# Kernel optimization log

Hardware: AMD Instinct MI355X
Metric: run time of the kernel (lower is better)

## Reference

```python
import jax, jax.numpy as jnp
import numpy as np
import math

EMBED_DIM = 1024
NUM_HEADS = 16
HEAD_DIM = EMBED_DIM // NUM_HEADS


def setup_inputs() -> dict:
    key = jax.random.key(0)
    ks = jax.random.split(key, 11)
    B, S, D = 4, 2048, EMBED_DIM
    scale = 1.0 / math.sqrt(D)
    inp = {
        'q': jax.random.normal(ks[0], (B, S, D), dtype=jnp.float32),
        'k': jax.random.normal(ks[1], (B, S, D), dtype=jnp.float32),
        'v': jax.random.normal(ks[2], (B, S, D), dtype=jnp.float32),
        'Wq': jax.random.normal(ks[3], (D, D), dtype=jnp.float32) * scale,
        'bq': jnp.zeros((D,), dtype=jnp.float32),
        'Wk': jax.random.normal(ks[4], (D, D), dtype=jnp.float32) * scale,
        'bk': jnp.zeros((D,), dtype=jnp.float32),
        'Wv': jax.random.normal(ks[5], (D, D), dtype=jnp.float32) * scale,
        'bv': jnp.zeros((D,), dtype=jnp.float32),
        'Wo': jax.random.normal(ks[6], (D, D), dtype=jnp.float32) * scale,
        'bo': jnp.zeros((D,), dtype=jnp.float32),
    }
    return inp


def reference(q, k, v, Wq, bq, Wk, bk, Wv, bv, Wo, bo):
    B, S, D = q.shape
    H, Hd = NUM_HEADS, HEAD_DIM
    # QKV projections (nn.Linear: x @ W.T + b), split into heads -> [B,H,S,Hd]
    qh = (q @ Wq.T + bq).reshape(B, S, H, Hd).transpose(0, 2, 1, 3)
    kh = (k @ Wk.T + bk).reshape(B, S, H, Hd).transpose(0, 2, 1, 3)
    vh = (v @ Wv.T + bv).reshape(B, S, H, Hd).transpose(0, 2, 1, 3)
    # Scaled dot-product attention, full [B,H,S,S] scores as in source
    scores = jnp.einsum('bhqd,bhkd->bhqk', qh, kh) / math.sqrt(Hd)
    probs = jax.nn.softmax(scores, axis=-1)
    attn = jnp.einsum('bhqk,bhkd->bhqd', probs, vh)
    # Merge heads and output projection
    concat = attn.transpose(0, 2, 1, 3).reshape(B, S, D)
    return concat @ Wo.T + bo
```

## Files before the change

kernel.cpp:

```cpp
#include <hip/hip_runtime.h>
#include <hip/hip_bf16.h>
#include <math.h>

#define D_MODEL 1024
#define NHEADS  16
#define HDIM    64
#define BATCH   4
#define SEQ     2048

typedef __attribute__((ext_vector_type(8))) short short8;
typedef __attribute__((ext_vector_type(4))) float f32x4;

__device__ __forceinline__ short bf16_of(float f) {
  __hip_bfloat16 h = __float2bfloat16(f);
  return *reinterpret_cast<short*>(&h);
}

__device__ __forceinline__ unsigned pack2(float lo, float hi) {
  return (unsigned)(unsigned short)bf16_of(lo) |
         ((unsigned)(unsigned short)bf16_of(hi) << 16);
}

__device__ __forceinline__ short8 mk_frag(unsigned a, unsigned b, unsigned c, unsigned d) {
  union { unsigned u[4]; short8 s; } t;
  t.u[0] = a; t.u[1] = b; t.u[2] = c; t.u[3] = d;
  return t.s;
}

__device__ __forceinline__ float fast_exp2(float x) {
  float r;
  asm("v_exp_f32 %0, %1" : "=v"(r) : "v"(x));
  return r;
}

__device__ __forceinline__ void gload16(const void* g, void* l) {
  __builtin_amdgcn_global_load_lds((const __attribute__((address_space(1))) void*)g,
                                   (__attribute__((address_space(3))) void*)l, 16, 0, 0);
}

__global__ __launch_bounds__(256) void cvt7(
    const float* __restrict__ Wq, const float* __restrict__ Wk,
    const float* __restrict__ Wv, const float* __restrict__ Wo,
    const float* __restrict__ q,  const float* __restrict__ k,
    const float* __restrict__ v,
    short* __restrict__ wdst, short* __restrict__ qc,
    short* __restrict__ kc,   short* __restrict__ vc)
{
  const int w = blockIdx.y;
  const float* s;
  short* d;
  int n4;
  if (w < 4) {
    s = (w == 0) ? Wq : (w == 1) ? Wk : (w == 2) ? Wv : Wo;
    d = wdst + (size_t)w * D_MODEL * D_MODEL;
    n4 = D_MODEL * D_MODEL / 4;
  } else {
    s = (w == 4) ? q : (w == 5) ? k : v;
    d = (w == 4) ? qc : (w == 5) ? kc : vc;
    n4 = BATCH * SEQ * D_MODEL / 4;
  }
  int stride = gridDim.x * blockDim.x;
  for (int i = blockIdx.x * blockDim.x + threadIdx.x; i < n4; i += stride) {
    float4 fv = reinterpret_cast<const float4*>(s)[i];
    reinterpret_cast<uint2*>(d)[i] = make_uint2(pack2(fv.x, fv.y), pack2(fv.z, fv.w));
  }
}

__global__ __launch_bounds__(256) void qkv_gemm(
    const short* __restrict__ qc, const short* __restrict__ kc, const short* __restrict__ vc,
    const short* __restrict__ Wqkv,
    const float* __restrict__ bq, const float* __restrict__ bk, const float* __restrict__ bv,
    short* __restrict__ Qb, short* __restrict__ Kb, short* __restrict__ Vb)
{
  const int tid  = threadIdx.x;
  const int lane = tid & 63;
  const int wave = tid >> 6;
  const int Lb  = blockIdx.x + 24 * blockIdx.y;
  const int xcd = Lb & 7;
  const int sl  = Lb >> 3;
  const int bx  = sl % 24;
  const int by  = (sl / 24) * 8 + xcd;

  const int sel = bx >> 3;
  const short* A    = (sel == 0) ? qc : (sel == 1) ? kc : vc;
  const float* bias = (sel == 0) ? bq : (sel == 1) ? bk : bv;
  short* Out        = (sel == 0) ? Qb : (sel == 1) ? Kb : Vb;
  const int m0  = by * 128;
  const int n0g = bx * 128;
  const int n0  = n0g & 1023;
  const int wm = (wave >> 1) * 64;
  const int wn = (wave & 1) * 64;

  __shared__ short As[128 * 32];
  __shared__ short Bs[128 * 32];

  f32x4 acc[4][4];
#pragma unroll
  for (int m = 0; m < 4; ++m)
#pragma unroll
    for (int n = 0; n < 4; ++n)
      acc[m][n] = (f32x4){0.f, 0.f, 0.f, 0.f};

  for (int k0 = 0; k0 < D_MODEL; k0 += 32) {
#pragma unroll
    for (int i = 0; i < 2; ++i) {
      int t = i * 256 + wave * 64 + lane;
      int row = t >> 2, c8 = (t & 3) * 8;
      gload16(&A[(size_t)(m0 + row) * D_MODEL + k0 + c8],    &As[i * 2048 + wave * 512]);
      gload16(&Wqkv[(size_t)(n0g + row) * D_MODEL + k0 + c8], &Bs[i * 2048 + wave * 512]);
    }
    __syncthreads();

    short8 afr[4], bfr[4];
#pragma unroll
    for (int m = 0; m < 4; ++m)
      afr[m] = *reinterpret_cast<const short8*>(&As[(wm + m * 16 + (lane & 15)) * 32 + (lane >> 4) * 8]);
#pragma unroll
    for (int n = 0; n < 4; ++n)
      bfr[n] = *reinterpret_cast<const short8*>(&Bs[(wn + n * 16 + (lane & 15)) * 32 + (lane >> 4) * 8]);
#pragma unroll
    for (int m = 0; m < 4; ++m)
#pragma unroll
      for (int n = 0; n < 4; ++n)
        acc[m][n] = __builtin_amdgcn_mfma_f32_16x16x32_bf16(afr[m], bfr[n], acc[m][n], 0, 0, 0);
    __syncthreads();
  }

#pragma unroll
  for (int n = 0; n < 4; ++n) {
    int col = n0 + wn + n * 16 + (lane & 15);
    float bval = bias[col];
#pragma unroll
    for (int m = 0; m < 4; ++m) {
      int rowb = m0 + wm + m * 16 + (lane >> 4) * 4;
#pragma unroll
      for (int r = 0; r < 4; ++r)
        Out[(size_t)(rowb + r) * D_MODEL + col] = bf16_of(acc[m][n][r] + bval);
    }
  }
}

__global__ __launch_bounds__(256) void gemm_out(
    const short* __restrict__ A, const short* __restrict__ Bw,
    const float* __restrict__ bias, float* __restrict__ Out,
    int M, int N, int K)
{
  const int tid  = threadIdx.x;
  const int lane = tid & 63;
  const int wave = tid >> 6;
  const int Lb  = blockIdx.x + 8 * blockIdx.y;
  const int xcd = Lb & 7;
  const int sl  = Lb >> 3;
  const int bx  = sl & 7;
  const int by  = (sl >> 3) * 8 + xcd;
  const int m0 = by * 128;
  const int n0 = bx * 128;
  const int wm = (wave >> 1) * 64;
  const int wn = (wave & 1) * 64;

  __shared__ short As[128 * 32];
  __shared__ short Bs[128 * 32];

  f32x4 acc[4][4];
#pragma unroll
  for (int m = 0; m < 4; ++m)
#pragma unroll
    for (int n = 0; n < 4; ++n)
      acc[m][n] = (f32x4){0.f, 0.f, 0.f, 0.f};

  for (int k0 = 0; k0 < K; k0 += 32) {
#pragma unroll
    for (int i = 0; i < 2; ++i) {
      int t = i * 256 + wave * 64 + lane;
      int row = t >> 2, c8 = (t & 3) * 8;
      gload16(&A[(size_t)(m0 + row) * K + k0 + c8],  &As[i * 2048 + wave * 512]);
      gload16(&Bw[(size_t)(n0 + row) * K + k0 + c8], &Bs[i * 2048 + wave * 512]);
    }
    __syncthreads();

    short8 afr[4], bfr[4];
#pragma unroll
    for (int m = 0; m < 4; ++m)
      afr[m] = *reinterpret_cast<const short8*>(&As[(wm + m * 16 + (lane & 15)) * 32 + (lane >> 4) * 8]);
#pragma unroll
    for (int n = 0; n < 4; ++n)
      bfr[n] = *reinterpret_cast<const short8*>(&Bs[(wn + n * 16 + (lane & 15)) * 32 + (lane >> 4) * 8]);
#pragma unroll
    for (int m = 0; m < 4; ++m)
#pragma unroll
      for (int n = 0; n < 4; ++n)
        acc[m][n] = __builtin_amdgcn_mfma_f32_16x16x32_bf16(afr[m], bfr[n], acc[m][n], 0, 0, 0);
    __syncthreads();
  }

#pragma unroll
  for (int n = 0; n < 4; ++n) {
    int col = n0 + wn + n * 16 + (lane & 15);
    float bval = bias[col];
#pragma unroll
    for (int m = 0; m < 4; ++m) {
      int rowb = m0 + wm + m * 16 + (lane >> 4) * 4;
#pragma unroll
      for (int r = 0; r < 4; ++r)
        Out[(size_t)(rowb + r) * N + col] = acc[m][n][r] + bval;
    }
  }
}

__global__ __launch_bounds__(256) void transpose_v(const short* __restrict__ V,
                                                   short* __restrict__ VT) {
  int st = blockIdx.x;
  int bh = blockIdx.y;
  int b = bh >> 4, h = bh & 15;
  __shared__ short T[64][72];
  int tid = threadIdx.x;
#pragma unroll
  for (int i = 0; i < 2; ++i) {
    int c = tid + i * 256;
    int srow = c >> 3;
    int d8 = (c & 7) * 8;
    *reinterpret_cast<uint4*>(&T[srow][d8]) = *reinterpret_cast<const uint4*>(
        &V[((size_t)b * SEQ + st * 64 + srow) * D_MODEL + h * HDIM + d8]);
  }
  __syncthreads();
#pragma unroll
  for (int i = 0; i < 2; ++i) {
    int c = tid + i * 256;
    int drow = c >> 3;
    int s8 = (c & 7) * 8;
    __align__(16) short tmp[8];
#pragma unroll
    for (int j = 0; j < 8; ++j) tmp[j] = T[s8 + j][drow];
    *reinterpret_cast<uint4*>(
        &VT[(((size_t)b * NHEADS + h) * HDIM + drow) * SEQ + st * 64 + s8]) =
        *reinterpret_cast<uint4*>(tmp);
  }
}

__global__ __launch_bounds__(512) void attn_fwd(
    const short* __restrict__ Q,
    const short* __restrict__ Kg,
    const short* __restrict__ VT,
    short* __restrict__ Oc)
{
  const int tid = threadIdx.x, lane = tid & 63, wave = tid >> 6;
  const int qi = lane & 15, g = lane >> 4;
  const int q0 = blockIdx.x * 128;
  const int bh = blockIdx.y, b = bh >> 4, h = bh & 15;

  __shared__ short Ks[2][64][72];
  __shared__ short Vs[2][64][72];

  const float CEXP = 0.18033688f;
  const float SMC  = 14.4269504f;
  const short8 ones = mk_frag(0x3F803F80u, 0x3F803F80u, 0x3F803F80u, 0x3F803F80u);

  short8 qfr[2];
  {
    int qrow = q0 + wave * 16 + qi;
    const short* qp = &Q[((size_t)b * SEQ + qrow) * D_MODEL + h * HDIM + g * 8];
    qfr[0] = *reinterpret_cast<const short8*>(qp);
    qfr[1] = *reinterpret_cast<const short8*>(qp + 32);
  }

  const size_t kbase = ((size_t)b * SEQ) * D_MODEL + h * HDIM;
  const size_t vbase = ((size_t)bh * HDIM) * SEQ;

  f32x4 o[4], o_l;
#pragma unroll
  for (int db = 0; db < 4; ++db) o[db] = (f32x4){0.f, 0.f, 0.f, 0.f};
  o_l = (f32x4){0.f, 0.f, 0.f, 0.f};

  {
    int row = tid >> 3, sub = tid & 7;
    *reinterpret_cast<uint4*>(&Ks[0][row][sub * 8]) =
        *reinterpret_cast<const uint4*>(&Kg[kbase + (size_t)row * D_MODEL + sub * 8]);
    uint4 vv = *reinterpret_cast<const uint4*>(&VT[vbase + (size_t)row * SEQ + sub * 8]);
    int posA = 32 * (sub >> 2) + 16 * (sub & 1) + 4 * ((sub >> 1) & 1);
    *reinterpret_cast<uint2*>(&Vs[0][row][posA])     = make_uint2(vv.x, vv.y);
    *reinterpret_cast<uint2*>(&Vs[0][row][posA + 8]) = make_uint2(vv.z, vv.w);
  }
  __syncthreads();

  for (int t = 0; t < SEQ / 64; ++t) {
    const int cur = t & 1;
    const bool more = (t + 1) < SEQ / 64;
    const int row = tid >> 3, sub = tid & 7;
    uint4 kreg, vreg;
    if (more) {
      int k0 = (t + 1) * 64;
      kreg = *reinterpret_cast<const uint4*>(&Kg[kbase + (size_t)(k0 + row) * D_MODEL + sub * 8]);
      vreg = *reinterpret_cast<const uint4*>(&VT[vbase + (size_t)row * SEQ + k0 + sub * 8]);
    }

    f32x4 st[4];
    __builtin_amdgcn_s_setprio(1);
#pragma unroll
    for (int n = 0; n < 4; ++n) {
      short8 a0 = *reinterpret_cast<const short8*>(&Ks[cur][n * 16 + qi][g * 8]);
      short8 a1 = *reinterpret_cast<const short8*>(&Ks[cur][n * 16 + qi][32 + g * 8]);
      f32x4 z = (f32x4){0.f, 0.f, 0.f, 0.f};
      z = __builtin_amdgcn_mfma_f32_16x16x32_bf16(a0, qfr[0], z, 0, 0, 0);
      z = __builtin_amdgcn_mfma_f32_16x16x32_bf16(a1, qfr[1], z, 0, 0, 0);
      st[n] = z;
    }
    __builtin_amdgcn_s_setprio(0);

    unsigned pk[4][2];
#pragma unroll
    for (int n = 0; n < 4; ++n) {
#pragma unroll
      for (int r = 0; r < 4; ++r)
        st[n][r] = fast_exp2(fmaf(st[n][r], CEXP, -SMC));
      pk[n][0] = pack2(st[n][0], st[n][1]);
      pk[n][1] = pack2(st[n][2], st[n][3]);
    }

    if (more) {
      const int nb = cur ^ 1;
      *reinterpret_cast<uint4*>(&Ks[nb][row][sub * 8]) = kreg;
      int posA = 32 * (sub >> 2) + 16 * (sub & 1) + 4 * ((sub >> 1) & 1);
      *reinterpret_cast<uint2*>(&Vs[nb][row][posA])     = make_uint2(vreg.x, vreg.y);
      *reinterpret_cast<uint2*>(&Vs[nb][row][posA + 8]) = make_uint2(vreg.z, vreg.w);
    }

    short8 pb0 = mk_frag(pk[0][0], pk[0][1], pk[1][0], pk[1][1]);
    short8 pb1 = mk_frag(pk[2][0], pk[2][1], pk[3][0], pk[3][1]);
    __builtin_amdgcn_s_setprio(1);
#pragma unroll
    for (int db = 0; db < 4; ++db) {
      short8 va0 = *reinterpret_cast<const short8*>(&Vs[cur][db * 16 + qi][g * 8]);
      short8 va1 = *reinterpret_cast<const short8*>(&Vs[cur][db * 16 + qi][32 + g * 8]);
      o[db] = __builtin_amdgcn_mfma_f32_16x16x32_bf16(va0, pb0, o[db], 0, 0, 0);
      o[db] = __builtin_amdgcn_mfma_f32_16x16x32_bf16(va1, pb1, o[db], 0, 0, 0);
    }
    o_l = __builtin_amdgcn_mfma_f32_16x16x32_bf16(ones, pb0, o_l, 0, 0, 0);
    o_l = __builtin_amdgcn_mfma_f32_16x16x32_bf16(ones, pb1, o_l, 0, 0, 0);
    __builtin_amdgcn_s_setprio(0);

    __syncthreads();
  }

  short (*Os)[72] = reinterpret_cast<short(*)[72]>(&Ks[0][0][0]);
  float inv = 1.f / o_l[0];
#pragma unroll
  for (int db = 0; db < 4; ++db)
#pragma unroll
    for (int r = 0; r < 4; ++r)
      Os[wave * 16 + qi][db * 16 + g * 4 + r] = bf16_of(o[db][r] * inv);
  __syncthreads();
#pragma unroll
  for (int i = 0; i < 2; ++i) {
    int c = tid + i * 512;
    int row = c >> 3, sub = c & 7;
    *reinterpret_cast<uint4*>(&Oc[((size_t)b * SEQ + q0 + row) * D_MODEL + h * HDIM + sub * 8]) =
        *reinterpret_cast<const uint4*>(&Os[row][sub * 8]);
  }
}

extern "C" void kernel_launch(void* const* d_in, const int* in_sizes, int n_in,
                              void* d_out, int out_size, void* d_ws, size_t ws_size,
                              hipStream_t stream)
{
  const float* q  = (const float*)d_in[0];
  const float* k  = (const float*)d_in[1];
  const float* v  = (const float*)d_in[2];
  const float* Wq = (const float*)d_in[3];
  const float* bq = (const float*)d_in[4];
  const float* Wk = (const float*)d_in[5];
  const float* bk = (const float*)d_in[6];
  const float* Wv = (const float*)d_in[7];
  const float* bv = (const float*)d_in[8];
  const float* Wo = (const float*)d_in[9];
  const float* bo = (const float*)d_in[10];

  char* ws = (char*)d_ws;
  const size_t MB = 1ull << 20;
  short* Wqkv_b = (short*)(ws + 0 * MB);
  short* Wo_b   = (short*)(ws + 6 * MB);
  short* Qb     = (short*)(ws + 8 * MB);
  short* Kb     = (short*)(ws + 24 * MB);
  short* Vb     = (short*)(ws + 40 * MB);
  short* qc     = (short*)(ws + 56 * MB);
  short* kc     = (short*)(ws + 72 * MB);
  short* vc     = (short*)(ws + 88 * MB);
  short* VTb    = (short*)(ws + 56 * MB);
  short* Ac     = (short*)(ws + 40 * MB);

  const int M = BATCH * SEQ;

  cvt7<<<dim3(256, 7), 256, 0, stream>>>(Wq, Wk, Wv, Wo, q, k, v, Wqkv_b, qc, kc, vc);

  qkv_gemm<<<dim3(24, M / 128), 256, 0, stream>>>(qc, kc, vc, Wqkv_b, bq, bk, bv, Qb, Kb, Vb);

  transpose_v<<<dim3(SEQ / 64, BATCH * NHEADS), 256, 0, stream>>>(Vb, VTb);

  attn_fwd<<<dim3(SEQ / 128, BATCH * NHEADS), 512, 0, stream>>>(Qb, Kb, VTb, Ac);

  gemm_out<<<dim3(D_MODEL / 128, M / 128), 256, 0, stream>>>(Ac, Wo_b, bo, (float*)d_out,
                                                             M, D_MODEL, D_MODEL);
}
```

Before: 219.4 us.

## Fuse V transpose into QKV GEMM epilogue and reorder attention schedule

The QKV GEMM epilogue now writes the V projection directly in the per-head transposed layout, which removes the separate transpose_v kernel and its extra pass over V. Attention blocks are remapped so blocks of the same batch-head land on the same XCD, for better L2 reuse of K/V. The softmax probabilities are packed with the hardware v_cvt_pk_bf16_f32 instruction, and the PV MFMAs are moved ahead of the LDS stores for the next tile. The transposed V stores are 8-byte scattered writes strided by SEQ, which may be less efficient than the old coalesced writes.

New measurement: 222.3 us. No clear change (+1.3%).

```diff
diff --git a/kernel.cpp b/kernel.cpp
--- a/kernel.cpp
+++ b/kernel.cpp
@@ -19,6 +19,12 @@
 __device__ __forceinline__ unsigned pack2(float lo, float hi) {
   return (unsigned)(unsigned short)bf16_of(lo) |
          ((unsigned)(unsigned short)bf16_of(hi) << 16);
+}
+
+__device__ __forceinline__ unsigned cvtpk(float lo, float hi) {
+  unsigned r;
+  asm("v_cvt_pk_bf16_f32 %0, %1, %2" : "=v"(r) : "v"(lo), "v"(hi));
+  return r;
 }
 
 __device__ __forceinline__ short8 mk_frag(unsigned a, unsigned b, unsigned c, unsigned d) {
@@ -70,7 +76,7 @@
     const short* __restrict__ qc, const short* __restrict__ kc, const short* __restrict__ vc,
     const short* __restrict__ Wqkv,
     const float* __restrict__ bq, const float* __restrict__ bk, const float* __restrict__ bv,
-    short* __restrict__ Qb, short* __restrict__ Kb, short* __restrict__ Vb)
+    short* __restrict__ Qb, short* __restrict__ Kb, short* __restrict__ VTb)
 {
   const int tid  = threadIdx.x;
   const int lane = tid & 63;
@@ -84,7 +90,6 @@
   const int sel = bx >> 3;
   const short* A    = (sel == 0) ? qc : (sel == 1) ? kc : vc;
   const float* bias = (sel == 0) ? bq : (sel == 1) ? bk : bv;
-  short* Out        = (sel == 0) ? Qb : (sel == 1) ? Kb : Vb;
   const int m0  = by * 128;
   const int n0g = bx * 128;
   const int n0  = n0g & 1023;
@@ -106,7 +111,7 @@
     for (int i = 0; i < 2; ++i) {
       int t = i * 256 + wave * 64 + lane;
       int row = t >> 2, c8 = (t & 3) * 8;
-      gload16(&A[(size_t)(m0 + row) * D_MODEL + k0 + c8],    &As[i * 2048 + wave * 512]);
+      gload16(&A[(size_t)(m0 + row) * D_MODEL + k0 + c8],     &As[i * 2048 + wave * 512]);
       gload16(&Wqkv[(size_t)(n0g + row) * D_MODEL + k0 + c8], &Bs[i * 2048 + wave * 512]);
     }
     __syncthreads();
@@ -126,16 +131,35 @@
     __syncthreads();
   }
 
-#pragma unroll
-  for (int n = 0; n < 4; ++n) {
-    int col = n0 + wn + n * 16 + (lane & 15);
-    float bval = bias[col];
-#pragma unroll
-    for (int m = 0; m < 4; ++m) {
-      int rowb = m0 + wm + m * 16 + (lane >> 4) * 4;
-#pragma unroll
-      for (int r = 0; r < 4; ++r)
-        Out[(size_t)(rowb + r) * D_MODEL + col] = bf16_of(acc[m][n][r] + bval);
+  if (sel < 2) {
+    short* Out = (sel == 0) ? Qb : Kb;
+#pragma unroll
+    for (int n = 0; n < 4; ++n) {
+      int col = n0 + wn + n * 16 + (lane & 15);
+      float bval = bias[col];
+#pragma unroll
+      for (int m = 0; m < 4; ++m) {
+        int rowb = m0 + wm + m * 16 + (lane >> 4) * 4;
+#pragma unroll
+        for (int r = 0; r < 4; ++r)
+          Out[(size_t)(rowb + r) * D_MODEL + col] = bf16_of(acc[m][n][r] + bval);
+      }
+    }
+  } else {
+#pragma unroll
+    for (int n = 0; n < 4; ++n) {
+      int col = n0 + wn + n * 16 + (lane & 15);
+      float bval = bias[col];
+      int h = col >> 6, d = col & 63;
+#pragma unroll
+      for (int m = 0; m < 4; ++m) {
+        int s0 = m0 + wm + m * 16 + (lane >> 4) * 4;
+        int b = s0 >> 11, sloc = s0 & 2047;
+        unsigned lo = pack2(acc[m][n][0] + bval, acc[m][n][1] + bval);
+        unsigned hi = pack2(acc[m][n][2] + bval, acc[m][n][3] + bval);
+        *reinterpret_cast<uint2*>(
+            &VTb[(((size_t)b * NHEADS + h) * HDIM + d) * SEQ + sloc]) = make_uint2(lo, hi);
+      }
     }
   }
 }
@@ -207,36 +231,6 @@
   }
 }
 
-__global__ __launch_bounds__(256) void transpose_v(const short* __restrict__ V,
-                                                   short* __restrict__ VT) {
-  int st = blockIdx.x;
-  int bh = blockIdx.y;
-  int b = bh >> 4, h = bh & 15;
-  __shared__ short T[64][72];
-  int tid = threadIdx.x;
-#pragma unroll
-  for (int i = 0; i < 2; ++i) {
-    int c = tid + i * 256;
-    int srow = c >> 3;
-    int d8 = (c & 7) * 8;
-    *reinterpret_cast<uint4*>(&T[srow][d8]) = *reinterpret_cast<const uint4*>(
-        &V[((size_t)b * SEQ + st * 64 + srow) * D_MODEL + h * HDIM + d8]);
-  }
-  __syncthreads();
-#pragma unroll
-  for (int i = 0; i < 2; ++i) {
-    int c = tid + i * 256;
-    int drow = c >> 3;
-    int s8 = (c & 7) * 8;
-    __align__(16) short tmp[8];
-#pragma unroll
-    for (int j = 0; j < 8; ++j) tmp[j] = T[s8 + j][drow];
-    *reinterpret_cast<uint4*>(
-        &VT[(((size_t)b * NHEADS + h) * HDIM + drow) * SEQ + st * 64 + s8]) =
-        *reinterpret_cast<uint4*>(tmp);
-  }
-}
-
 __global__ __launch_bounds__(512) void attn_fwd(
     const short* __restrict__ Q,
     const short* __restrict__ Kg,
@@ -245,8 +239,13 @@
 {
   const int tid = threadIdx.x, lane = tid & 63, wave = tid >> 6;
   const int qi = lane & 15, g = lane >> 4;
-  const int q0 = blockIdx.x * 128;
-  const int bh = blockIdx.y, b = bh >> 4, h = bh & 15;
+  const int Lb  = blockIdx.x + 16 * blockIdx.y;
+  const int xcd = Lb & 7;
+  const int slot = Lb >> 3;
+  const int bh  = (slot >> 4) * 8 + xcd;
+  const int qblk = slot & 15;
+  const int q0 = qblk * 128;
+  const int b = bh >> 4, h = bh & 15;
 
   __shared__ short Ks[2][64][72];
   __shared__ short Vs[2][64][72];
@@ -312,9 +311,23 @@
 #pragma unroll
       for (int r = 0; r < 4; ++r)
         st[n][r] = fast_exp2(fmaf(st[n][r], CEXP, -SMC));
-      pk[n][0] = pack2(st[n][0], st[n][1]);
-      pk[n][1] = pack2(st[n][2], st[n][3]);
-    }
+      pk[n][0] = cvtpk(st[n][0], st[n][1]);
+      pk[n][1] = cvtpk(st[n][2], st[n][3]);
+    }
+
+    short8 pb0 = mk_frag(pk[0][0], pk[0][1], pk[1][0], pk[1][1]);
+    short8 pb1 = mk_frag(pk[2][0], pk[2][1], pk[3][0], pk[3][1]);
+    __builtin_amdgcn_s_setprio(1);
+#pragma unroll
+    for (int db = 0; db < 4; ++db) {
+      short8 va0 = *reinterpret_cast<const short8*>(&Vs[cur][db * 16 + qi][g * 8]);
+      short8 va1 = *reinterpret_cast<const short8*>(&Vs[cur][db * 16 + qi][32 + g * 8]);
+      o[db] = __builtin_amdgcn_mfma_f32_16x16x32_bf16(va0, pb0, o[db], 0, 0, 0);
+      o[db] = __builtin_amdgcn_mfma_f32_16x16x32_bf16(va1, pb1, o[db], 0, 0, 0);
+    }
+    o_l = __builtin_amdgcn_mfma_f32_16x16x32_bf16(ones, pb0, o_l, 0, 0, 0);
+    o_l = __builtin_amdgcn_mfma_f32_16x16x32_bf16(ones, pb1, o_l, 0, 0, 0);
+    __builtin_amdgcn_s_setprio(0);
 
     if (more) {
       const int nb = cur ^ 1;
@@ -323,20 +336,6 @@
       *reinterpret_cast<uint2*>(&Vs[nb][row][posA])     = make_uint2(vreg.x, vreg.y);
       *reinterpret_cast<uint2*>(&Vs[nb][row][posA + 8]) = make_uint2(vreg.z, vreg.w);
     }
-
-    short8 pb0 = mk_frag(pk[0][0], pk[0][1], pk[1][0], pk[1][1]);
-    short8 pb1 = mk_frag(pk[2][0], pk[2][1], pk[3][0], pk[3][1]);
-    __builtin_amdgcn_s_setprio(1);
-#pragma unroll
-    for (int db = 0; db < 4; ++db) {
-      short8 va0 = *reinterpret_cast<const short8*>(&Vs[cur][db * 16 + qi][g * 8]);
-      short8 va1 = *reinterpret_cast<const short8*>(&Vs[cur][db * 16 + qi][32 + g * 8]);
-      o[db] = __builtin_amdgcn_mfma_f32_16x16x32_bf16(va0, pb0, o[db], 0, 0, 0);
-      o[db] = __builtin_amdgcn_mfma_f32_16x16x32_bf16(va1, pb1, o[db], 0, 0, 0);
-    }
-    o_l = __builtin_amdgcn_mfma_f32_16x16x32_bf16(ones, pb0, o_l, 0, 0, 0);
-    o_l = __builtin_amdgcn_mfma_f32_16x16x32_bf16(ones, pb1, o_l, 0, 0, 0);
-    __builtin_amdgcn_s_setprio(0);
 
     __syncthreads();
   }
@@ -380,20 +379,17 @@
   short* Wo_b   = (short*)(ws + 6 * MB);
   short* Qb     = (short*)(ws + 8 * MB);
   short* Kb     = (short*)(ws + 24 * MB);
-  short* Vb     = (short*)(ws + 40 * MB);
+  short* VTb    = (short*)(ws + 40 * MB);
   short* qc     = (short*)(ws + 56 * MB);
   short* kc     = (short*)(ws + 72 * MB);
   short* vc     = (short*)(ws + 88 * MB);
-  short* VTb    = (short*)(ws + 56 * MB);
-  short* Ac     = (short*)(ws + 40 * MB);
+  short* Ac     = (short*)(ws + 56 * MB);
 
   const int M = BATCH * SEQ;
 
   cvt7<<<dim3(256, 7), 256, 0, stream>>>(Wq, Wk, Wv, Wo, q, k, v, Wqkv_b, qc, kc, vc);
 
-  qkv_gemm<<<dim3(24, M / 128), 256, 0, stream>>>(qc, kc, vc, Wqkv_b, bq, bk, bv, Qb, Kb, Vb);
-
-  transpose_v<<<dim3(SEQ / 64, BATCH * NHEADS), 256, 0, stream>>>(Vb, VTb);
+  qkv_gemm<<<dim3(24, M / 128), 256, 0, stream>>>(qc, kc, vc, Wqkv_b, bq, bk, bv, Qb, Kb, VTb);
 
   attn_fwd<<<dim3(SEQ / 128, BATCH * NHEADS), 512, 0, stream>>>(Qb, Kb, VTb, Ac);
 
```
